# Optimization experiments

Measured on AMD Instinct MI355X. Metric: run time of the kernel, lower is better.

Reference implementation:

```python
import jax, jax.numpy as jnp
import numpy as np

PUSH_MARGIN = 0.25


def setup_inputs() -> dict:
    key = jax.random.key(0)
    k1, k2 = jax.random.split(key)
    B, H, W, D, K = 8, 512, 512, 32, 64
    embeddings = jax.random.normal(k1, (B, H, W, D), dtype=jnp.float32)
    labels = jax.random.randint(k2, (B, H, W), 0, K, dtype=jnp.int32)
    return {"embeddings": embeddings, "labels": labels, "n_instances": K}


def _metric_loss(embeddings, labels, n_instances):
    # embeddings: (B, H, W, D) float; labels: (B, H, W) int; n_instances: static int K
    B = embeddings.shape[0]
    D = embeddings.shape[-1]
    K = n_instances
    emb = embeddings.reshape(B, -1, D)          # (B, N, D)
    lab = labels.reshape(B, -1).astype(jnp.int32)  # (B, N)

    # One-pass segment reduce over all batches: offset labels per batch element.
    seg = (lab + jnp.arange(B, dtype=jnp.int32)[:, None] * K).reshape(-1)  # (B*N,)
    sums = jax.ops.segment_sum(emb.reshape(-1, D), seg, num_segments=B * K)
    counts = jax.ops.segment_sum(jnp.ones(seg.shape, dtype=emb.dtype), seg,
                                 num_segments=B * K)
    sums = sums.reshape(B, K, D)
    counts = counts.reshape(B, K)
    present = counts > 0.5                       # non-empty instances (B, K)
    centroids = sums / jnp.maximum(counts, 1.0)[..., None]  # (B, K, D); zeros if empty

    # Pairwise Manhattan distances between centroids: (B, K, K)
    dist = jnp.sum(jnp.abs(centroids[:, :, None, :] - centroids[:, None, :, :]), axis=-1)
    hinge = jax.nn.relu(PUSH_MARGIN - dist)      # push: relu(margin - d)
    sq = hinge * hinge                           # squared error metric

    # strictly upper triangular + only pairs of non-empty instances
    triu = jnp.triu(jnp.ones((K, K), dtype=bool), k=1)
    pair_mask = triu[None] & present[:, :, None] & present[:, None, :]
    per_image_sum = jnp.sum(jnp.where(pair_mask, sq, 0.0), axis=(1, 2))  # (B,)

    n = jnp.sum(present.astype(emb.dtype), axis=1)              # (B,) non-empty count
    n_comparisons = n * (n - 1.0) / 2.0
    push_loss = per_image_sum / n_comparisons
    return jnp.mean(push_loss)


def reference(embeddings, labels, n_instances):
    return _metric_loss(embeddings, labels, n_instances)
```

## Files before the change

### kernel.cpp

```cpp
#include <hip/hip_runtime.h>

#define B_    8
#define N_    (512 * 512)
#define D_    32
#define K_    64
#define TPB   256
#define NWAVE (TPB / 64)
#define KROW  36
#define TABW  (K_ * KROW)
#define REC   (K_ * D_ + K_)
#define RECQ  (REC / 4)

#define PROC(L0,L1,L2,L3,L4,L5,L6,L7, V, PBASE)                               \
  {                                                                           \
    int lb = egl < 4 ? (egl < 2 ? (egl == 0 ? L0 : L1)                        \
                                : (egl == 2 ? L2 : L3))                       \
                     : (egl < 6 ? (egl == 4 ? L4 : L5)                        \
                                : (egl == 6 ? L6 : L7));                      \
    const int m0 = (lb == L0), m1 = (lb == L1), m2 = (lb == L2),              \
              m3 = (lb == L3), m4 = (lb == L4), m5 = (lb == L5),              \
              m6 = (lb == L6), m7 = (lb == L7);                               \
    const int order = (g0 & m0) + (g1 & m1) + (g2 & m2) + (g3 & m3) +         \
                      (g4 & m4) + (g5 & m5) + (g6 & m6);                      \
    const int nsame = m0 + m1 + m2 + m3 + m4 + m5 + m6 + m7;                  \
    const float4 vc = V;                                                      \
    const int pb = (PBASE);                                                   \
    if (pb < iend) {                  \
      const int* lp = lab + bbase + pb + wb;      \
      L0 = lp[0]; L1 = lp[1]; L2 = lp[2]; L3 = lp[3];                         \
      L4 = lp[4]; L5 = lp[5]; L6 = lp[6]; L7 = lp[7];                         \
      V = embv[(bbase + pb + eg) * 8 + d4];                                   \
    }                                                                         \
    const int a = lb * KROW + d4 * 4;                                         \
    if (order == 0) {                                                         \
      float4 cur = *reinterpret_cast<const float4*>(tab + a);                 \
      cur.x += vc.x; cur.y += vc.y; cur.z += vc.z; cur.w += vc.w;             \
      *reinterpret_cast<float4*>(tab + a) = cur;                              \
      if (d4 == 0) cnt[lb] += (float)nsame;                                   \
    } else {                  \
      atomicAdd(&tab[a + 0], vc.x);                                           \
      atomicAdd(&tab[a + 1], vc.y);                                           \
      atomicAdd(&tab[a + 2], vc.z);                                           \
      atomicAdd(&tab[a + 3], vc.w);                                           \
    }                                                                         \
  }

__global__ __launch_bounds__(TPB) void seg_partial_kernel(
    const float* __restrict__ emb, const int* __restrict__ lab,
    float* __restrict__ partials, int blk_per_b)
{
    __shared__ __align__(16) float s_tab[NWAVE * TABW];
    __shared__ float s_cnt[NWAVE * K_];

    for (int i = threadIdx.x; i < NWAVE * TABW; i += TPB) s_tab[i] = 0.f;
    for (int i = threadIdx.x; i < NWAVE * K_;  i += TPB) s_cnt[i] = 0.f;
    __syncthreads();

    const int tid  = threadIdx.x;
    const int wave = tid >> 6;
    const int lane = tid & 63;
    const int egl  = lane >> 3;
    const int d4   = lane & 7;
    const int eg   = wave * 8 + egl;

    const int g0 = (0 < egl), g1 = (1 < egl), g2 = (2 < egl), g3 = (3 < egl),
              g4 = (4 < egl), g5 = (5 < egl), g6 = (6 < egl);

    float* __restrict__ tab = s_tab + wave * TABW;
    float* __restrict__ cnt = s_cnt + wave * K_;

    const int blk = blockIdx.x;
    const int b   = blk / blk_per_b;
    const int bib = blk - b * blk_per_b;
    const long long bbase = (long long)b * N_;
    const float4* __restrict__ embv = reinterpret_cast<const float4*>(emb);
    const int CHUNK = N_ / blk_per_b;
    const int wb = __builtin_amdgcn_readfirstlane(wave * 8);

    int ib = bib * CHUNK;
    const int iend = ib + CHUNK;

    int a0, a1, a2, a3, a4, a5, a6, a7;
    float4 va;
    {
        const int* lp = lab + bbase + ib + wb;
        a0 = lp[0]; a1 = lp[1]; a2 = lp[2]; a3 = lp[3];
        a4 = lp[4]; a5 = lp[5]; a6 = lp[6]; a7 = lp[7];
        va = embv[(bbase + ib + eg) * 8 + d4];
    }
    int b0 = 0, b1 = 0, b2 = 0, b3 = 0, b4 = 0, b5 = 0, b6 = 0, b7 = 0;
    float4 vb = make_float4(0.f, 0.f, 0.f, 0.f);
    if (ib + 32 < iend) {
        const int* lp = lab + bbase + ib + 32 + wb;
        b0 = lp[0]; b1 = lp[1]; b2 = lp[2]; b3 = lp[3];
        b4 = lp[4]; b5 = lp[5]; b6 = lp[6]; b7 = lp[7];
        vb = embv[(bbase + ib + 32 + eg) * 8 + d4];
    }

    for (;;) {
        PROC(a0, a1, a2, a3, a4, a5, a6, a7, va, ib + 64);
        ib += 32;
        if (ib >= iend) break;
        PROC(b0, b1, b2, b3, b4, b5, b6, b7, vb, ib + 64);
        ib += 32;
        if (ib >= iend) break;
    }
    __syncthreads();

    float* out = partials + (size_t)blk * REC;
    for (int i = tid; i < K_ * D_; i += TPB) {
        int k = i >> 5, d = i & 31;
        float s = 0.f;
#pragma unroll
        for (int w = 0; w < NWAVE; ++w) s += s_tab[w * TABW + k * KROW + d];
        out[i] = s;
    }
    if (tid < K_) {
        float c = 0.f;
#pragma unroll
        for (int w = 0; w < NWAVE; ++w) c += s_cnt[w * K_ + tid];
        out[K_ * D_ + tid] = c;
    }
}

__global__ __launch_bounds__(TPB) void seg_reduce_a(
    const float* __restrict__ partials, float* __restrict__ part2,
    int rpc, int nch)
{
    const int blk = blockIdx.x;
    const int b   = blk / nch;
    const int ch  = blk - b * nch;
    const int tid = threadIdx.x;

    const float4* __restrict__ p4 = reinterpret_cast<const float4*>(partials)
        + (size_t)((b * nch + ch) * rpc) * RECQ;
    float4* __restrict__ o4 = reinterpret_cast<float4*>(part2)
        + (size_t)blk * RECQ;

    float4 acc0 = make_float4(0.f, 0.f, 0.f, 0.f);
    float4 acc1 = acc0, acc2 = acc0;
#pragma unroll 4
    for (int r = 0; r < rpc; ++r) {
        const float4* rp = p4 + (size_t)r * RECQ;
        float4 v0 = rp[tid];
        float4 v1 = rp[tid + 256];
        acc0.x += v0.x; acc0.y += v0.y; acc0.z += v0.z; acc0.w += v0.w;
        acc1.x += v1.x; acc1.y += v1.y; acc1.z += v1.z; acc1.w += v1.w;
        if (tid < 16) {
            float4 v2 = rp[tid + 512];
            acc2.x += v2.x; acc2.y += v2.y; acc2.z += v2.z; acc2.w += v2.w;
        }
    }
    o4[tid]       = acc0;
    o4[tid + 256] = acc1;
    if (tid < 16) o4[tid + 512] = acc2;
}

__global__ __launch_bounds__(TPB) void loss8_kernel(
    const float* __restrict__ part2, float* __restrict__ batch_loss,
    int nch)
{
    __shared__ __align__(16) float4 s_cent4[8 * K_];
    __shared__ float s_cntsh[K_];
    __shared__ float s_pres[K_];
    __shared__ float s_wred[NWAVE];

    const int b   = blockIdx.x;
    const int tid = threadIdx.x;
    const float4* __restrict__ p4 = reinterpret_cast<const float4*>(part2)
        + (size_t)(b * nch) * RECQ;

    float4 acc0 = make_float4(0.f, 0.f, 0.f, 0.f);
    float4 acc1 = acc0, acc2 = acc0;
#pragma unroll 8
    for (int c = 0; c < nch; ++c) {
        const float4* rp = p4 + (size_t)c * RECQ;
        float4 v0 = rp[tid];
        float4 v1 = rp[tid + 256];
        acc0.x += v0.x; acc0.y += v0.y; acc0.z += v0.z; acc0.w += v0.w;
        acc1.x += v1.x; acc1.y += v1.y; acc1.z += v1.z; acc1.w += v1.w;
        if (tid < 16) {
            float4 v2 = rp[tid + 512];
            acc2.x += v2.x; acc2.y += v2.y; acc2.z += v2.z; acc2.w += v2.w;
        }
    }

    s_cent4[(tid & 7) * K_ + (tid >> 3)] = acc0;
    {
        const int q1 = tid + 256;
        s_cent4[(q1 & 7) * K_ + (q1 >> 3)] = acc1;
    }
    if (tid < 16) reinterpret_cast<float4*>(s_cntsh)[tid] = acc2;
    __syncthreads();

    if (tid < K_) s_pres[tid] = (s_cntsh[tid] > 0.5f) ? 1.f : 0.f;
    for (int i = tid; i < 8 * K_; i += TPB) {
        float inv = 1.0f / fmaxf(s_cntsh[i & 63], 1.0f);
        float4 c = s_cent4[i];
        c.x *= inv; c.y *= inv; c.z *= inv; c.w *= inv;
        s_cent4[i] = c;
    }
    __syncthreads();

    const int wave = tid >> 6, lane = tid & 63;

    float4 cb[8];
#pragma unroll
    for (int j = 0; j < 8; ++j) cb[j] = s_cent4[j * K_ + lane];
    const float pres2 = s_pres[lane];

    float acc = 0.f;
#pragma unroll 4
    for (int t = 0; t < 16; ++t) {
        const int k1 = wave * 16 + t;
        float dist = 0.f;
#pragma unroll
        for (int j = 0; j < 8; ++j) {
            float4 a = s_cent4[j * K_ + k1];
            dist += fabsf(a.x - cb[j].x) + fabsf(a.y - cb[j].y)
                  + fabsf(a.z - cb[j].z) + fabsf(a.w - cb[j].w);
        }
        float h = fmaxf(0.25f - dist, 0.f);
        float valid = (k1 < lane) ? s_pres[k1] * pres2 : 0.f;
        acc += valid * h * h;
    }
#pragma unroll
    for (int m = 32; m > 0; m >>= 1) acc += __shfl_xor(acc, m);
    if (lane == 0) s_wred[wave] = acc;
    __syncthreads();
    if (tid == 0) {
        float s = s_wred[0] + s_wred[1] + s_wred[2] + s_wred[3];
        float n = 0.f;
        for (int k = 0; k < K_; ++k) n += s_pres[k];
        float ncomp = n * (n - 1.f) * 0.5f;
        batch_loss[b] = (ncomp > 0.f) ? (s / ncomp) : 0.f;
    }
}

__global__ void final_kernel(const float* __restrict__ batch_loss,
                             float* __restrict__ out)
{
    if (threadIdx.x == 0) {
        float t = 0.f;
#pragma unroll
        for (int b = 0; b < B_; ++b) t += batch_loss[b];
        out[0] = t * (1.0f / (float)B_);
    }
}

extern "C" void kernel_launch(void* const* d_in, const int* in_sizes, int n_in,
                              void* d_out, int out_size, void* d_ws, size_t ws_size,
                              hipStream_t stream)
{
    const float* emb = (const float*)d_in[0];
    const int*   lab = (const int*)d_in[1];
    float*       out = (float*)d_out;
    float*       ws  = (float*)d_ws;

    int blk_per_b = 128;
    while (blk_per_b > 8) {
        size_t need = ((size_t)(blk_per_b * B_) * REC
                       + (size_t)(B_ * 8) * REC
                       + B_) * sizeof(float);
        if (need <= ws_size) break;
        blk_per_b >>= 1;
    }
    const int nblk = blk_per_b * B_;
    const int nch  = (blk_per_b >= 8) ? 8 : blk_per_b;
    const int rpc  = blk_per_b / nch;

    float* partials   = ws;
    float* part2      = ws + (size_t)nblk * REC;
    float* batch_loss = part2 + (size_t)(B_ * nch) * REC;

    seg_partial_kernel<<<nblk, TPB, 0, stream>>>(emb, lab, partials, blk_per_b);

    seg_reduce_a<<<B_ * nch, TPB, 0, stream>>>(partials, part2, rpc, nch);

    loss8_kernel<<<B_, TPB, 0, stream>>>(part2, batch_loss, nch);

    final_kernel<<<1, 64, 0, stream>>>(batch_loss, out);
}
```

Before: 76.36 us.

## Stage label segments in shared memory before per-wave accumulation

Labels are now loaded into a shared-memory buffer in 512-element segments with coalesced int4 loads, then read from LDS inside the accumulation loop instead of as scalar global loads. The goal is to replace redundant per-lane global label reads with one cooperative load. In exchange, each segment needs two block-wide barriers, and the software prefetch pipeline restarts at every segment boundary, which could stall the embedding loads.

Result: faster. 74.56 us (-2.4%).

```diff
diff --git a/kernel.cpp b/kernel.cpp
--- a/kernel.cpp
+++ b/kernel.cpp
@@ -10,6 +10,7 @@
 #define TABW  (K_ * KROW)
 #define REC   (K_ * D_ + K_)
 #define RECQ  (REC / 4)
+#define SEG   512
 
 #define PROC(L0,L1,L2,L3,L4,L5,L6,L7, V, PBASE)                               \
   {                                                                           \
@@ -25,11 +26,13 @@
     const int nsame = m0 + m1 + m2 + m3 + m4 + m5 + m6 + m7;                  \
     const float4 vc = V;                                                      \
     const int pb = (PBASE);                                                   \
-    if (pb < iend) {                  \
-      const int* lp = lab + bbase + pb + wb;      \
-      L0 = lp[0]; L1 = lp[1]; L2 = lp[2]; L3 = lp[3];                         \
-      L4 = lp[4]; L5 = lp[5]; L6 = lp[6]; L7 = lp[7];                         \
-      V = embv[(bbase + pb + eg) * 8 + d4];                                   \
+    if (pb < send) {                      \
+      const int4* lq = reinterpret_cast<const int4*>(s_lab + (pb - sbeg) + wb);\
+      int4 u0 = lq[0];              \
+      int4 u1 = lq[1];                                                        \
+      L0 = u0.x; L1 = u0.y; L2 = u0.z; L3 = u0.w;                             \
+      L4 = u1.x; L5 = u1.y; L6 = u1.z; L7 = u1.w;                             \
+      V = embv[(bbase + pb + eg) * 8 + d4];         \
     }                                                                         \
     const int a = lb * KROW + d4 * 4;                                         \
     if (order == 0) {                                                         \
@@ -51,10 +54,10 @@
 {
     __shared__ __align__(16) float s_tab[NWAVE * TABW];
     __shared__ float s_cnt[NWAVE * K_];
+    __shared__ __align__(16) int s_lab[SEG];
 
     for (int i = threadIdx.x; i < NWAVE * TABW; i += TPB) s_tab[i] = 0.f;
     for (int i = threadIdx.x; i < NWAVE * K_;  i += TPB) s_cnt[i] = 0.f;
-    __syncthreads();
 
     const int tid  = threadIdx.x;
     const int wave = tid >> 6;
@@ -77,33 +80,48 @@
     const int CHUNK = N_ / blk_per_b;
     const int wb = __builtin_amdgcn_readfirstlane(wave * 8);
 
-    int ib = bib * CHUNK;
-    const int iend = ib + CHUNK;
-
-    int a0, a1, a2, a3, a4, a5, a6, a7;
-    float4 va;
-    {
-        const int* lp = lab + bbase + ib + wb;
-        a0 = lp[0]; a1 = lp[1]; a2 = lp[2]; a3 = lp[3];
-        a4 = lp[4]; a5 = lp[5]; a6 = lp[6]; a7 = lp[7];
-        va = embv[(bbase + ib + eg) * 8 + d4];
-    }
-    int b0 = 0, b1 = 0, b2 = 0, b3 = 0, b4 = 0, b5 = 0, b6 = 0, b7 = 0;
-    float4 vb = make_float4(0.f, 0.f, 0.f, 0.f);
-    if (ib + 32 < iend) {
-        const int* lp = lab + bbase + ib + 32 + wb;
-        b0 = lp[0]; b1 = lp[1]; b2 = lp[2]; b3 = lp[3];
-        b4 = lp[4]; b5 = lp[5]; b6 = lp[6]; b7 = lp[7];
-        vb = embv[(bbase + ib + 32 + eg) * 8 + d4];
-    }
-
-    for (;;) {
-        PROC(a0, a1, a2, a3, a4, a5, a6, a7, va, ib + 64);
-        ib += 32;
-        if (ib >= iend) break;
-        PROC(b0, b1, b2, b3, b4, b5, b6, b7, vb, ib + 64);
-        ib += 32;
-        if (ib >= iend) break;
+    const int cstart = bib * CHUNK;
+    const int cend   = cstart + CHUNK;
+
+    for (int sbeg = cstart; sbeg < cend; sbeg += SEG) {
+        const int send = (sbeg + SEG < cend) ? sbeg + SEG : cend;
+        __syncthreads();
+        {
+            const int nq = (send - sbeg) >> 2;
+            const int4* gq = reinterpret_cast<const int4*>(lab + bbase + sbeg);
+            int4* sq = reinterpret_cast<int4*>(s_lab);
+            for (int q = tid; q < nq; q += TPB) sq[q] = gq[q];
+        }
+        __syncthreads();
+
+        int ib = sbeg;
+        int a0, a1, a2, a3, a4, a5, a6, a7;
+        float4 va;
+        {
+            const int4* lq = reinterpret_cast<const int4*>(s_lab + (ib - sbeg) + wb);
+            int4 u0 = lq[0], u1 = lq[1];
+            a0 = u0.x; a1 = u0.y; a2 = u0.z; a3 = u0.w;
+            a4 = u1.x; a5 = u1.y; a6 = u1.z; a7 = u1.w;
+            va = embv[(bbase + ib + eg) * 8 + d4];
+        }
+        int b0 = 0, b1 = 0, b2 = 0, b3 = 0, b4 = 0, b5 = 0, b6 = 0, b7 = 0;
+        float4 vb = make_float4(0.f, 0.f, 0.f, 0.f);
+        if (ib + 32 < send) {
+            const int4* lq = reinterpret_cast<const int4*>(s_lab + (ib + 32 - sbeg) + wb);
+            int4 u0 = lq[0], u1 = lq[1];
+            b0 = u0.x; b1 = u0.y; b2 = u0.z; b3 = u0.w;
+            b4 = u1.x; b5 = u1.y; b6 = u1.z; b7 = u1.w;
+            vb = embv[(bbase + ib + 32 + eg) * 8 + d4];
+        }
+
+        for (;;) {
+            PROC(a0, a1, a2, a3, a4, a5, a6, a7, va, ib + 64);
+            ib += 32;
+            if (ib >= send) break;
+            PROC(b0, b1, b2, b3, b4, b5, b6, b7, vb, ib + 64);
+            ib += 32;
+            if (ib >= send) break;
+        }
     }
     __syncthreads();
 
```
